# Kernel optimization log

Hardware: AMD Instinct MI355X
Metric: run time of the kernel (lower is better)

## Reference

```python
import jax, jax.numpy as jnp
import numpy as np

EMBED = 1024
HEADS = 16
HEAD_DIM = EMBED // HEADS
MAX_REL = 8
B, S = 4, 1024


def setup_inputs() -> dict:
    key = jax.random.key(0)
    ks = jax.random.split(key, 12)
    lim = 1.0 / np.sqrt(EMBED)
    def lin(k):
        k1, k2 = jax.random.split(k)
        W = jax.random.uniform(k1, (EMBED, EMBED), jnp.float32, -lim, lim)
        b = jax.random.uniform(k2, (EMBED,), jnp.float32, -lim, lim)
        return W, b
    Wq, bq = lin(ks[0]); Wk, bk = lin(ks[1]); Wv, bv = lin(ks[2]); Wo, bo = lin(ks[3])
    return {
        'query': jax.random.normal(ks[4], (B, S, EMBED), jnp.float32),
        'key': jax.random.normal(ks[5], (B, S, EMBED), jnp.float32),
        'value': jax.random.normal(ks[6], (B, S, EMBED), jnp.float32),
        'mask': jnp.zeros((B, S, S), dtype=bool),
        'Wq': Wq, 'bq': bq, 'Wk': Wk, 'bk': bk, 'Wv': Wv, 'bv': bv,
        'Wo': Wo, 'bo': bo,
        'rel_bias': jnp.zeros((HEADS, 2 * MAX_REL + 1), jnp.float32),
    }


def _split_heads(x):
    b, s, _ = x.shape
    return x.reshape(b, s, HEADS, HEAD_DIM).transpose(0, 2, 1, 3)  # [b,h,s,d]


def reference(query, key, value, mask, Wq, bq, Wk, bk, Wv, bv, Wo, bo, rel_bias):
    scale = jnp.sqrt(jnp.float32(HEAD_DIM))
    Q = _split_heads(query @ Wq.T + bq)
    K = _split_heads(key @ Wk.T + bk)
    V = _split_heads(value @ Wv.T + bv)
    scores = jnp.einsum('bhqd,bhkd->bhqk', Q, K) / scale
    # relative position bias: rel_bias[h, clip(j-i)+max]
    idx = jnp.arange(query.shape[1])
    rel = jnp.clip(idx[None, :] - idx[:, None], -MAX_REL, MAX_REL) + MAX_REL  # [s,s]
    bias = rel_bias[:, rel]  # [h,s,s]
    scores = scores + bias[None]
    scores = jnp.where(mask[:, None, :, :], -jnp.inf, scores)
    attn = jax.nn.softmax(scores, axis=-1)
    ctx = jnp.einsum('bhqk,bhkd->bhqd', attn, V)
    b, h, s, d = ctx.shape
    out = ctx.transpose(0, 2, 1, 3).reshape(b, s, h * d) @ Wo.T + bo
    return out, attn, scores
```

## Files before the change

kernel.cpp:

```cpp
#include <hip/hip_runtime.h>

typedef __bf16 bf16_t;
typedef bf16_t bf16x4 __attribute__((ext_vector_type(4)));
typedef bf16_t bf16x8 __attribute__((ext_vector_type(8)));
typedef float f32x4 __attribute__((ext_vector_type(4)));
typedef float f32x8 __attribute__((ext_vector_type(8)));

#define B_N 4
#define S_N 1024
#define E_N 1024
#define H_N 16
#define D_N 64

#define MFMA16 __builtin_amdgcn_mfma_f32_16x16x32_bf16

static __device__ __forceinline__ bf16_t f2b(float x) { return (bf16_t)x; }

static __device__ __forceinline__ void gload_lds16(const void* g, void* l) {
  __builtin_amdgcn_global_load_lds(
      (const __attribute__((address_space(1))) unsigned int*)g,
      (__attribute__((address_space(3))) unsigned int*)l, 16, 0, 0);
}

__global__ __launch_bounds__(256) void convert_kernel(
    const float* __restrict__ q, const float* __restrict__ k, const float* __restrict__ v,
    const float* __restrict__ wq, const float* __restrict__ wk,
    const float* __restrict__ wv, const float* __restrict__ wo,
    bf16_t* __restrict__ dq, bf16_t* __restrict__ dk, bf16_t* __restrict__ dv,
    bf16_t* __restrict__ dwq, bf16_t* __restrict__ dwk,
    bf16_t* __restrict__ dwv, bf16_t* __restrict__ dwo)
{
  const size_t e = ((size_t)blockIdx.x * 256 + threadIdx.x) * 8;
  const float* src; bf16_t* dst; size_t off;
  if (e < 12582912ull) {
    const int which = (int)(e >> 22);
    off = e & 4194303ull;
    src = which == 0 ? q : (which == 1 ? k : v);
    dst = which == 0 ? dq : (which == 1 ? dk : dv);
  } else {
    const size_t e2 = e - 12582912ull;
    const int which = (int)(e2 >> 20);
    off = e2 & 1048575ull;
    src = which == 0 ? wq : (which == 1 ? wk : (which == 2 ? wv : wo));
    dst = which == 0 ? dwq : (which == 1 ? dwk : (which == 2 ? dwv : dwo));
  }
  f32x8 x = *(const f32x8*)(src + off);
  bf16x8 r;
#pragma unroll
  for (int i = 0; i < 8; ++i) r[i] = f2b(x[i]);
  *(bf16x8*)(dst + off) = r;
}

__global__ __launch_bounds__(256) void mask_rowany(
    const unsigned char* __restrict__ mask, unsigned char* __restrict__ flags)
{
  const int row = blockIdx.x * 4 + (threadIdx.x >> 6);
  const int lane = threadIdx.x & 63;
  const uint4 v = *(const uint4*)(mask + (size_t)row * 1024 + lane * 16);
  const unsigned int any = v.x | v.y | v.z | v.w;
  const unsigned long long bal = __ballot(any != 0);
  if (lane == 0) flags[row] = bal ? 1 : 0;
}

__global__ __launch_bounds__(256) void qkv_gemm(
    const bf16_t* __restrict__ qA, const bf16_t* __restrict__ kA, const bf16_t* __restrict__ vA,
    const bf16_t* __restrict__ Wq, const bf16_t* __restrict__ Wk, const bf16_t* __restrict__ Wv,
    const float* __restrict__ bq, const float* __restrict__ bk, const float* __restrict__ bv,
    bf16_t* __restrict__ Qo, bf16_t* __restrict__ Ko, bf16_t* __restrict__ Vto)
{
  const int z = blockIdx.z;
  const bf16_t* A = z == 0 ? qA : (z == 1 ? kA : vA);
  const bf16_t* W = z == 0 ? Wq : (z == 1 ? Wk : Wv);
  const float* bias = z == 0 ? bq : (z == 1 ? bk : bv);

  __shared__ bf16_t As[128 * 32];
  __shared__ bf16_t Bs[128 * 32];
  const int tid = threadIdx.x;
  const int m0 = blockIdx.y * 128, n0 = blockIdx.x * 128;
  const int lane = tid & 63, wid = tid >> 6;
  const int wr = wid >> 1, wc = wid & 1;
  const int lr = lane & 15, lh = lane >> 4;
  const int sr = lane >> 2, sc = (lane & 3) * 8;
  f32x4 acc[4][4] = {};
  for (int k0 = 0; k0 < 1024; k0 += 32) {
#pragma unroll
    for (int i = 0; i < 2; ++i) {
      const int br = wid * 32 + i * 16;
      gload_lds16(&A[(size_t)(m0 + br + sr) * 1024 + k0 + sc], &As[br * 32]);
      gload_lds16(&W[(size_t)(n0 + br + sr) * 1024 + k0 + sc], &Bs[br * 32]);
    }
    __syncthreads();
    bf16x8 af[4], bw[4];
#pragma unroll
    for (int m = 0; m < 4; ++m)
      af[m] = *(const bf16x8*)&As[(wr * 64 + m * 16 + lr) * 32 + lh * 8];
#pragma unroll
    for (int n = 0; n < 4; ++n)
      bw[n] = *(const bf16x8*)&Bs[(wc * 64 + n * 16 + lr) * 32 + lh * 8];
#pragma unroll
    for (int m = 0; m < 4; ++m)
#pragma unroll
      for (int n = 0; n < 4; ++n)
        acc[m][n] = MFMA16(af[m], bw[n], acc[m][n], 0, 0, 0);
    __syncthreads();
  }
#pragma unroll
  for (int n = 0; n < 4; ++n) {
    const int col = n0 + wc * 64 + n * 16 + lr;
    const float bv_ = bias[col];
    const int h = col >> 6, d = col & 63;
#pragma unroll
    for (int m = 0; m < 4; ++m) {
      const int row0 = m0 + wr * 64 + m * 16 + lh * 4;
#pragma unroll
      for (int r = 0; r < 4; ++r) {
        const int row = row0 + r;
        const float v = acc[m][n][r] + bv_;
        const int b = row >> 10, s = row & 1023;
        if (z == 0)
          Qo[((size_t)(b * H_N + h) * S_N + s) * D_N + d] = f2b(v);
        else if (z == 1)
          Ko[((size_t)(b * H_N + h) * S_N + s) * D_N + d] = f2b(v);
        else
          Vto[((size_t)(b * H_N + h) * D_N + d) * S_N + s] = f2b(v);
      }
    }
  }
}

__global__ __launch_bounds__(256) void out_gemm(
    const bf16_t* __restrict__ A, const bf16_t* __restrict__ W,
    const float* __restrict__ bias, float* __restrict__ Co)
{
  __shared__ bf16_t As[128 * 32];
  __shared__ bf16_t Bs[128 * 32];
  const int tid = threadIdx.x;
  const int m0 = blockIdx.y * 128, n0 = blockIdx.x * 128;
  const int lane = tid & 63, wid = tid >> 6;
  const int wr = wid >> 1, wc = wid & 1;
  const int lr = lane & 15, lh = lane >> 4;
  const int sr = lane >> 2, sc = (lane & 3) * 8;
  f32x4 acc[4][4] = {};
  for (int k0 = 0; k0 < 1024; k0 += 32) {
#pragma unroll
    for (int i = 0; i < 2; ++i) {
      const int br = wid * 32 + i * 16;
      gload_lds16(&A[(size_t)(m0 + br + sr) * 1024 + k0 + sc], &As[br * 32]);
      gload_lds16(&W[(size_t)(n0 + br + sr) * 1024 + k0 + sc], &Bs[br * 32]);
    }
    __syncthreads();
    bf16x8 af[4], bw[4];
#pragma unroll
    for (int m = 0; m < 4; ++m)
      af[m] = *(const bf16x8*)&As[(wr * 64 + m * 16 + lr) * 32 + lh * 8];
#pragma unroll
    for (int n = 0; n < 4; ++n)
      bw[n] = *(const bf16x8*)&Bs[(wc * 64 + n * 16 + lr) * 32 + lh * 8];
#pragma unroll
    for (int m = 0; m < 4; ++m)
#pragma unroll
      for (int n = 0; n < 4; ++n)
        acc[m][n] = MFMA16(af[m], bw[n], acc[m][n], 0, 0, 0);
    __syncthreads();
  }
#pragma unroll
  for (int n = 0; n < 4; ++n) {
    const int col = n0 + wc * 64 + n * 16 + lr;
    const float bv_ = bias[col];
#pragma unroll
    for (int m = 0; m < 4; ++m) {
      const int row0 = m0 + wr * 64 + m * 16 + lh * 4;
#pragma unroll
      for (int r = 0; r < 4; ++r)
        Co[(size_t)(row0 + r) * E_N + col] = acc[m][n][r] + bv_;
    }
  }
}

static __device__ __forceinline__ f32x4 score4(
    f32x4 acc, int qrow, int kc, const unsigned char* __restrict__ mrow,
    const float* __restrict__ rbh, float rb_lo, float rb_hi, bool um)
{
  const int d0 = kc - qrow;
  float b0, b1, b2, b3;
  if (d0 >= 8) { b0 = b1 = b2 = b3 = rb_hi; }
  else if (d0 <= -11) { b0 = b1 = b2 = b3 = rb_lo; }
  else {
    int dd;
    dd = d0;     dd = dd < -8 ? -8 : (dd > 8 ? 8 : dd); b0 = rbh[dd + 8];
    dd = d0 + 1; dd = dd < -8 ? -8 : (dd > 8 ? 8 : dd); b1 = rbh[dd + 8];
    dd = d0 + 2; dd = dd < -8 ? -8 : (dd > 8 ? 8 : dd); b2 = rbh[dd + 8];
    dd = d0 + 3; dd = dd < -8 ? -8 : (dd > 8 ? 8 : dd); b3 = rbh[dd + 8];
  }
  f32x4 s;
  s[0] = acc[0] * 0.125f + b0;
  s[1] = acc[1] * 0.125f + b1;
  s[2] = acc[2] * 0.125f + b2;
  s[3] = acc[3] * 0.125f + b3;
  if (um) {
    const unsigned int mw = *(const unsigned int*)(mrow + kc);
    const float NEG = -__builtin_inff();
    if (mw & 0xffu)       s[0] = NEG;
    if (mw & 0xff00u)     s[1] = NEG;
    if (mw & 0xff0000u)   s[2] = NEG;
    if (mw & 0xff000000u) s[3] = NEG;
  }
  return s;
}

__global__ __launch_bounds__(256) void fused_attn(
    const bf16_t* __restrict__ Q, const bf16_t* __restrict__ K,
    const bf16_t* __restrict__ Vt,
    const unsigned char* __restrict__ mask, const unsigned char* __restrict__ rowflag,
    const float* __restrict__ rel_bias,
    float* __restrict__ scores, float* __restrict__ attn, bf16_t* __restrict__ ctx)
{
  __shared__ bf16_t Ktile[64 * 64];
  __shared__ bf16_t Vtile[64 * 64];
  __shared__ float S_lds[4][16][68];

  const int bh = blockIdx.y, b = bh >> 4, h = bh & 15;
  const int q0 = blockIdx.x * 64;
  const int tid = threadIdx.x;
  const int w = tid >> 6, lane = tid & 63;
  const int lr = lane & 15, lh = lane >> 4;
  const int qrow = q0 + w * 16 + lr;

  const bf16_t* Qh = Q + (size_t)bh * (S_N * D_N);
  const bf16_t* Kh = K + (size_t)bh * (S_N * D_N);
  const bf16_t* Vh = Vt + (size_t)bh * (D_N * S_N);
  const unsigned char* mrow = mask + (size_t)b * S_N * S_N + (size_t)qrow * S_N;
  float* Sbase = scores + (size_t)bh * S_N * S_N + (size_t)(q0 + w * 16) * S_N;
  float* Abase = attn + (size_t)bh * S_N * S_N + (size_t)(q0 + w * 16) * S_N;
  const float* rbh = rel_bias + h * 17;
  const float rb_lo = rbh[0], rb_hi = rbh[16];
  const float NEG = -__builtin_inff();
  const bool um = rowflag[b * S_N + qrow] != 0;

  const int sg_row0 = tid >> 3, sg_c = tid & 7;
  const int sg_row1 = (tid + 256) >> 3;
  const int sg_s0 = (sg_c ^ (sg_row0 & 7)) * 8;
  const int sg_s1 = (sg_c ^ (sg_row1 & 7)) * 8;

  bf16x8 qa0 = *(const bf16x8*)&Qh[(size_t)qrow * D_N + lh * 8];
  bf16x8 qa1 = *(const bf16x8*)&Qh[(size_t)qrow * D_N + 32 + lh * 8];

  const int ks0 = (lh ^ (lr & 7)) * 8;
  const int ks1 = ((4 + lh) ^ (lr & 7)) * 8;

  float mrun = NEG, srun = 0.f;
  for (int kt = 0; kt < 16; ++kt) {
    const int kb = kt * 64;
    __syncthreads();
    *(bf16x8*)&Ktile[sg_row0 * 64 + sg_s0] =
        *(const bf16x8*)&Kh[(size_t)(kb + sg_row0) * D_N + sg_c * 8];
    *(bf16x8*)&Ktile[sg_row1 * 64 + sg_s1] =
        *(const bf16x8*)&Kh[(size_t)(kb + sg_row1) * D_N + sg_c * 8];
    __syncthreads();
#pragma unroll
    for (int t = 0; t < 4; ++t) {
      const int krow = t * 16 + lr;
      bf16x8 ka0 = *(const bf16x8*)&Ktile[krow * 64 + ks0];
      bf16x8 ka1 = *(const bf16x8*)&Ktile[krow * 64 + ks1];
      f32x4 acc = {};
      acc = MFMA16(ka0, qa0, acc, 0, 0, 0);
      acc = MFMA16(ka1, qa1, acc, 0, 0, 0);
      const int kc = kb + t * 16 + 4 * lh;
      f32x4 s = score4(acc, qrow, kc, mrow, rbh, rb_lo, rb_hi, um);
      *(f32x4*)&S_lds[w][lr][t * 16 + 4 * lh] = s;
      const float mt = fmaxf(fmaxf(s[0], s[1]), fmaxf(s[2], s[3]));
      const float mn = fmaxf(mrun, mt);
      if (mn > NEG) {
        srun = srun * __expf(mrun - mn)
             + __expf(s[0] - mn) + __expf(s[1] - mn)
             + __expf(s[2] - mn) + __expf(s[3] - mn);
        mrun = mn;
      }
    }
#pragma unroll
    for (int i = 0; i < 4; ++i) {
      const int row = 4 * i + lh;
      f32x4 sv = *(const f32x4*)&S_lds[w][row][lr * 4];
      *(f32x4*)&Sbase[(size_t)row * S_N + kb + lr * 4] = sv;
    }
  }
#pragma unroll
  for (int off = 16; off <= 32; off <<= 1) {
    const float m2 = __shfl_xor(mrun, off);
    const float s2 = __shfl_xor(srun, off);
    const float mn = fmaxf(mrun, m2);
    if (mn > NEG) {
      srun = srun * __expf(mrun - mn) + s2 * __expf(m2 - mn);
      mrun = mn;
    }
  }
  const float M = mrun;
  const float invs = 1.0f / srun;

  f32x4 accp[4] = {};
  for (int kt = 0; kt < 16; ++kt) {
    const int kb = kt * 64;
    __syncthreads();
    *(bf16x8*)&Ktile[sg_row0 * 64 + sg_s0] =
        *(const bf16x8*)&Kh[(size_t)(kb + sg_row0) * D_N + sg_c * 8];
    *(bf16x8*)&Ktile[sg_row1 * 64 + sg_s1] =
        *(const bf16x8*)&Kh[(size_t)(kb + sg_row1) * D_N + sg_c * 8];
    *(bf16x8*)&Vtile[sg_row0 * 64 + sg_s0] =
        *(const bf16x8*)&Vh[(size_t)sg_row0 * S_N + kb + sg_c * 8];
    *(bf16x8*)&Vtile[sg_row1 * 64 + sg_s1] =
        *(const bf16x8*)&Vh[(size_t)sg_row1 * S_N + kb + sg_c * 8];
    __syncthreads();
#pragma unroll
    for (int t = 0; t < 4; ++t) {
      const int krow = t * 16 + lr;
      bf16x8 ka0 = *(const bf16x8*)&Ktile[krow * 64 + ks0];
      bf16x8 ka1 = *(const bf16x8*)&Ktile[krow * 64 + ks1];
      f32x4 acc = {};
      acc = MFMA16(ka0, qa0, acc, 0, 0, 0);
      acc = MFMA16(ka1, qa1, acc, 0, 0, 0);
      const int kc = kb + t * 16 + 4 * lh;
      f32x4 s = score4(acc, qrow, kc, mrow, rbh, rb_lo, rb_hi, um);
      f32x4 p;
#pragma unroll
      for (int j = 0; j < 4; ++j) p[j] = __expf(s[j] - M) * invs;
      *(f32x4*)&S_lds[w][lr][t * 16 + 4 * lh] = p;
    }
#pragma unroll
    for (int i = 0; i < 4; ++i) {
      const int row = 4 * i + lh;
      f32x4 pv = *(const f32x4*)&S_lds[w][row][lr * 4];
      *(f32x4*)&Abase[(size_t)row * S_N + kb + lr * 4] = pv;
    }
#pragma unroll
    for (int ch = 0; ch < 2; ++ch) {
      f32x8 pf = *(const f32x8*)&S_lds[w][lr][ch * 32 + lh * 8];
      bf16x8 pa;
#pragma unroll
      for (int j = 0; j < 8; ++j) pa[j] = f2b(pf[j]);
#pragma unroll
      for (int dt = 0; dt < 4; ++dt) {
        const int drow = dt * 16 + lr;
        bf16x8 vb = *(const bf16x8*)&Vtile[drow * 64 + (((ch * 4 + lh) ^ (lr & 7)) * 8)];
        accp[dt] = MFMA16(pa, vb, accp[dt], 0, 0, 0);
      }
    }
  }
#pragma unroll
  for (int dt = 0; dt < 4; ++dt)
#pragma unroll
    for (int r = 0; r < 4; ++r)
      ctx[((size_t)(b * S_N + q0 + w * 16 + 4 * lh + r)) * E_N + h * 64 + dt * 16 + lr] =
          f2b(accp[dt][r]);
}

extern "C" void kernel_launch(void* const* d_in, const int* in_sizes, int n_in,
                              void* d_out, int out_size, void* d_ws, size_t ws_size,
                              hipStream_t stream) {
  (void)in_sizes; (void)n_in; (void)out_size; (void)ws_size;
  const float* query = (const float*)d_in[0];
  const float* key   = (const float*)d_in[1];
  const float* value = (const float*)d_in[2];
  const unsigned char* mask = (const unsigned char*)d_in[3];
  const float* Wq = (const float*)d_in[4];
  const float* bq = (const float*)d_in[5];
  const float* Wk = (const float*)d_in[6];
  const float* bk = (const float*)d_in[7];
  const float* Wv = (const float*)d_in[8];
  const float* bv = (const float*)d_in[9];
  const float* Wo = (const float*)d_in[10];
  const float* bo = (const float*)d_in[11];
  const float* rel_bias = (const float*)d_in[12];

  float* out_f    = (float*)d_out;
  float* attn_f   = out_f + (size_t)4194304;
  float* scores_f = attn_f + (size_t)67108864;

  char* ws = (char*)d_ws;
  bf16_t* qbf  = (bf16_t*)(ws);
  bf16_t* kbf  = (bf16_t*)(ws + (8ull  << 20));
  bf16_t* vbf  = (bf16_t*)(ws + (16ull << 20));
  bf16_t* Wqb  = (bf16_t*)(ws + (24ull << 20));
  bf16_t* Wkb  = (bf16_t*)(ws + (26ull << 20));
  bf16_t* Wvb  = (bf16_t*)(ws + (28ull << 20));
  bf16_t* Wob  = (bf16_t*)(ws + (30ull << 20));
  bf16_t* Qbf  = (bf16_t*)(ws + (32ull << 20));
  bf16_t* Kbf  = (bf16_t*)(ws + (40ull << 20));
  bf16_t* Vtbf = (bf16_t*)(ws + (48ull << 20));
  bf16_t* CTX  = (bf16_t*)(ws + (56ull << 20));
  unsigned char* FLAGS = (unsigned char*)(ws + (64ull << 20));

  convert_kernel<<<dim3(8192), dim3(256), 0, stream>>>(
      query, key, value, Wq, Wk, Wv, Wo, qbf, kbf, vbf, Wqb, Wkb, Wvb, Wob);
  mask_rowany<<<dim3(1024), dim3(256), 0, stream>>>(mask, FLAGS);
  qkv_gemm<<<dim3(8, 32, 3), dim3(256), 0, stream>>>(
      qbf, kbf, vbf, Wqb, Wkb, Wvb, bq, bk, bv, Qbf, Kbf, Vtbf);
  fused_attn<<<dim3(16, 64), dim3(256), 0, stream>>>(
      Qbf, Kbf, Vtbf, mask, FLAGS, rel_bias, scores_f, attn_f, CTX);
  out_gemm<<<dim3(8, 32), dim3(256), 0, stream>>>(CTX, Wob, bo, out_f);
}
```

Baseline: 241.6 us.

## Switch attention to single-pass online softmax with lazy rescale and separate normalization

The two-pass fused attention, which recomputed QK^T in a second pass, becomes a single flash-style pass. That pass writes raw scores, accumulates P·V using an online max that only rescales when the max grows past a threshold, and stores per-row max and inverse-sum statistics. A new elementwise kernel then reads scores back and writes the normalized attention matrix. K and V tiles are now double-buffered with register prefetch two tiles ahead. This removes the second QK^T compute and the second K/V pass, but adds a full re-read of the 64M-float scores tensor and an extra launch. The unnormalized exponentials can reach up to e^8 before rescaling, which is a bf16 precision risk.

```diff
diff --git a/kernel.cpp b/kernel.cpp
--- a/kernel.cpp
+++ b/kernel.cpp
@@ -208,15 +208,15 @@
   return s;
 }
 
-__global__ __launch_bounds__(256) void fused_attn(
+__global__ __launch_bounds__(256) void attn_pass1(
     const bf16_t* __restrict__ Q, const bf16_t* __restrict__ K,
     const bf16_t* __restrict__ Vt,
     const unsigned char* __restrict__ mask, const unsigned char* __restrict__ rowflag,
     const float* __restrict__ rel_bias,
-    float* __restrict__ scores, float* __restrict__ attn, bf16_t* __restrict__ ctx)
-{
-  __shared__ bf16_t Ktile[64 * 64];
-  __shared__ bf16_t Vtile[64 * 64];
+    float* __restrict__ scores, float2* __restrict__ stats, bf16_t* __restrict__ ctx)
+{
+  __shared__ bf16_t Kt[2][64 * 64];
+  __shared__ bf16_t Vtl[2][64 * 64];
   __shared__ float S_lds[4][16][68];
 
   const int bh = blockIdx.y, b = bh >> 4, h = bh & 15;
@@ -231,14 +231,14 @@
   const bf16_t* Vh = Vt + (size_t)bh * (D_N * S_N);
   const unsigned char* mrow = mask + (size_t)b * S_N * S_N + (size_t)qrow * S_N;
   float* Sbase = scores + (size_t)bh * S_N * S_N + (size_t)(q0 + w * 16) * S_N;
-  float* Abase = attn + (size_t)bh * S_N * S_N + (size_t)(q0 + w * 16) * S_N;
   const float* rbh = rel_bias + h * 17;
   const float rb_lo = rbh[0], rb_hi = rbh[16];
   const float NEG = -__builtin_inff();
+  const float THR = 8.0f;
   const bool um = rowflag[b * S_N + qrow] != 0;
 
   const int sg_row0 = tid >> 3, sg_c = tid & 7;
-  const int sg_row1 = (tid + 256) >> 3;
+  const int sg_row1 = sg_row0 + 32;
   const int sg_s0 = (sg_c ^ (sg_row0 & 7)) * 8;
   const int sg_s1 = (sg_c ^ (sg_row1 & 7)) * 8;
 
@@ -248,34 +248,52 @@
   const int ks0 = (lh ^ (lr & 7)) * 8;
   const int ks1 = ((4 + lh) ^ (lr & 7)) * 8;
 
+  bf16x8 kr0, kr1, vr0, vr1;
+  kr0 = *(const bf16x8*)&Kh[(size_t)sg_row0 * D_N + sg_c * 8];
+  kr1 = *(const bf16x8*)&Kh[(size_t)sg_row1 * D_N + sg_c * 8];
+  vr0 = *(const bf16x8*)&Vh[(size_t)sg_row0 * S_N + sg_c * 8];
+  vr1 = *(const bf16x8*)&Vh[(size_t)sg_row1 * S_N + sg_c * 8];
+  *(bf16x8*)&Kt[0][sg_row0 * 64 + sg_s0] = kr0;
+  *(bf16x8*)&Kt[0][sg_row1 * 64 + sg_s1] = kr1;
+  *(bf16x8*)&Vtl[0][sg_row0 * 64 + sg_s0] = vr0;
+  *(bf16x8*)&Vtl[0][sg_row1 * 64 + sg_s1] = vr1;
+  kr0 = *(const bf16x8*)&Kh[(size_t)(64 + sg_row0) * D_N + sg_c * 8];
+  kr1 = *(const bf16x8*)&Kh[(size_t)(64 + sg_row1) * D_N + sg_c * 8];
+  vr0 = *(const bf16x8*)&Vh[(size_t)sg_row0 * S_N + 64 + sg_c * 8];
+  vr1 = *(const bf16x8*)&Vh[(size_t)sg_row1 * S_N + 64 + sg_c * 8];
+  __syncthreads();
+
   float mrun = NEG, srun = 0.f;
-  for (int kt = 0; kt < 16; ++kt) {
-    const int kb = kt * 64;
-    __syncthreads();
-    *(bf16x8*)&Ktile[sg_row0 * 64 + sg_s0] =
-        *(const bf16x8*)&Kh[(size_t)(kb + sg_row0) * D_N + sg_c * 8];
-    *(bf16x8*)&Ktile[sg_row1 * 64 + sg_s1] =
-        *(const bf16x8*)&Kh[(size_t)(kb + sg_row1) * D_N + sg_c * 8];
-    __syncthreads();
-#pragma unroll
-    for (int t = 0; t < 4; ++t) {
-      const int krow = t * 16 + lr;
-      bf16x8 ka0 = *(const bf16x8*)&Ktile[krow * 64 + ks0];
-      bf16x8 ka1 = *(const bf16x8*)&Ktile[krow * 64 + ks1];
+  f32x4 accp[4] = {};
+
+  for (int t = 0; t < 16; ++t) {
+    const int cur = t & 1, kb = t * 64;
+    if (t + 1 < 16) {
+      *(bf16x8*)&Kt[cur ^ 1][sg_row0 * 64 + sg_s0] = kr0;
+      *(bf16x8*)&Kt[cur ^ 1][sg_row1 * 64 + sg_s1] = kr1;
+      *(bf16x8*)&Vtl[cur ^ 1][sg_row0 * 64 + sg_s0] = vr0;
+      *(bf16x8*)&Vtl[cur ^ 1][sg_row1 * 64 + sg_s1] = vr1;
+    }
+    if (t + 2 < 16) {
+      const int kb2 = (t + 2) * 64;
+      kr0 = *(const bf16x8*)&Kh[(size_t)(kb2 + sg_row0) * D_N + sg_c * 8];
+      kr1 = *(const bf16x8*)&Kh[(size_t)(kb2 + sg_row1) * D_N + sg_c * 8];
+      vr0 = *(const bf16x8*)&Vh[(size_t)sg_row0 * S_N + kb2 + sg_c * 8];
+      vr1 = *(const bf16x8*)&Vh[(size_t)sg_row1 * S_N + kb2 + sg_c * 8];
+    }
+    float mt = NEG;
+#pragma unroll
+    for (int t4 = 0; t4 < 4; ++t4) {
+      const int krow = t4 * 16 + lr;
+      bf16x8 ka0 = *(const bf16x8*)&Kt[cur][krow * 64 + ks0];
+      bf16x8 ka1 = *(const bf16x8*)&Kt[cur][krow * 64 + ks1];
       f32x4 acc = {};
       acc = MFMA16(ka0, qa0, acc, 0, 0, 0);
       acc = MFMA16(ka1, qa1, acc, 0, 0, 0);
-      const int kc = kb + t * 16 + 4 * lh;
+      const int kc = kb + t4 * 16 + 4 * lh;
       f32x4 s = score4(acc, qrow, kc, mrow, rbh, rb_lo, rb_hi, um);
-      *(f32x4*)&S_lds[w][lr][t * 16 + 4 * lh] = s;
-      const float mt = fmaxf(fmaxf(s[0], s[1]), fmaxf(s[2], s[3]));
-      const float mn = fmaxf(mrun, mt);
-      if (mn > NEG) {
-        srun = srun * __expf(mrun - mn)
-             + __expf(s[0] - mn) + __expf(s[1] - mn)
-             + __expf(s[2] - mn) + __expf(s[3] - mn);
-        mrun = mn;
-      }
+      *(f32x4*)&S_lds[w][lr][t4 * 16 + 4 * lh] = s;
+      mt = fmaxf(mt, fmaxf(fmaxf(s[0], s[1]), fmaxf(s[2], s[3])));
     }
 #pragma unroll
     for (int i = 0; i < 4; ++i) {
@@ -283,74 +301,73 @@
       f32x4 sv = *(const f32x4*)&S_lds[w][row][lr * 4];
       *(f32x4*)&Sbase[(size_t)row * S_N + kb + lr * 4] = sv;
     }
-  }
-#pragma unroll
-  for (int off = 16; off <= 32; off <<= 1) {
-    const float m2 = __shfl_xor(mrun, off);
-    const float s2 = __shfl_xor(srun, off);
-    const float mn = fmaxf(mrun, m2);
-    if (mn > NEG) {
-      srun = srun * __expf(mrun - mn) + s2 * __expf(m2 - mn);
-      mrun = mn;
-    }
-  }
-  const float M = mrun;
-  const float invs = 1.0f / srun;
-
-  f32x4 accp[4] = {};
-  for (int kt = 0; kt < 16; ++kt) {
-    const int kb = kt * 64;
-    __syncthreads();
-    *(bf16x8*)&Ktile[sg_row0 * 64 + sg_s0] =
-        *(const bf16x8*)&Kh[(size_t)(kb + sg_row0) * D_N + sg_c * 8];
-    *(bf16x8*)&Ktile[sg_row1 * 64 + sg_s1] =
-        *(const bf16x8*)&Kh[(size_t)(kb + sg_row1) * D_N + sg_c * 8];
-    *(bf16x8*)&Vtile[sg_row0 * 64 + sg_s0] =
-        *(const bf16x8*)&Vh[(size_t)sg_row0 * S_N + kb + sg_c * 8];
-    *(bf16x8*)&Vtile[sg_row1 * 64 + sg_s1] =
-        *(const bf16x8*)&Vh[(size_t)sg_row1 * S_N + kb + sg_c * 8];
-    __syncthreads();
-#pragma unroll
-    for (int t = 0; t < 4; ++t) {
-      const int krow = t * 16 + lr;
-      bf16x8 ka0 = *(const bf16x8*)&Ktile[krow * 64 + ks0];
-      bf16x8 ka1 = *(const bf16x8*)&Ktile[krow * 64 + ks1];
-      f32x4 acc = {};
-      acc = MFMA16(ka0, qa0, acc, 0, 0, 0);
-      acc = MFMA16(ka1, qa1, acc, 0, 0, 0);
-      const int kc = kb + t * 16 + 4 * lh;
-      f32x4 s = score4(acc, qrow, kc, mrow, rbh, rb_lo, rb_hi, um);
-      f32x4 p;
-#pragma unroll
-      for (int j = 0; j < 4; ++j) p[j] = __expf(s[j] - M) * invs;
-      *(f32x4*)&S_lds[w][lr][t * 16 + 4 * lh] = p;
-    }
-#pragma unroll
-    for (int i = 0; i < 4; ++i) {
-      const int row = 4 * i + lh;
-      f32x4 pv = *(const f32x4*)&S_lds[w][row][lr * 4];
-      *(f32x4*)&Abase[(size_t)row * S_N + kb + lr * 4] = pv;
-    }
+    mt = fmaxf(mt, __shfl_xor(mt, 16));
+    mt = fmaxf(mt, __shfl_xor(mt, 32));
+    if (__any(mt - mrun > THR)) {
+      const float mnew = fmaxf(mrun, mt);
+      const float sc = (mnew > NEG) ? ((mrun > NEG) ? __expf(mrun - mnew) : 0.f) : 1.f;
+      srun *= sc;
+      mrun = mnew;
+#pragma unroll
+      for (int r = 0; r < 4; ++r) {
+        const float fr = __shfl(sc, 4 * lh + r);
+#pragma unroll
+        for (int dt = 0; dt < 4; ++dt) accp[dt][r] *= fr;
+      }
+    }
+    const bool live = mrun > NEG;
 #pragma unroll
     for (int ch = 0; ch < 2; ++ch) {
       f32x8 pf = *(const f32x8*)&S_lds[w][lr][ch * 32 + lh * 8];
       bf16x8 pa;
 #pragma unroll
-      for (int j = 0; j < 8; ++j) pa[j] = f2b(pf[j]);
+      for (int j = 0; j < 8; ++j) {
+        const float e = live ? __expf(pf[j] - mrun) : 0.f;
+        srun += e;
+        pa[j] = f2b(e);
+      }
 #pragma unroll
       for (int dt = 0; dt < 4; ++dt) {
         const int drow = dt * 16 + lr;
-        bf16x8 vb = *(const bf16x8*)&Vtile[drow * 64 + (((ch * 4 + lh) ^ (lr & 7)) * 8)];
+        bf16x8 vb = *(const bf16x8*)&Vtl[cur][drow * 64 + (((ch * 4 + lh) ^ (lr & 7)) * 8)];
         accp[dt] = MFMA16(pa, vb, accp[dt], 0, 0, 0);
       }
     }
-  }
+    __syncthreads();
+  }
+
+  srun += __shfl_xor(srun, 16);
+  srun += __shfl_xor(srun, 32);
+  const float invs = srun > 0.f ? 1.0f / srun : 0.f;
+  if (lane < 16)
+    stats[(size_t)bh * S_N + q0 + w * 16 + lr] = make_float2(mrun, invs);
 #pragma unroll
   for (int dt = 0; dt < 4; ++dt)
 #pragma unroll
-    for (int r = 0; r < 4; ++r)
+    for (int r = 0; r < 4; ++r) {
+      const float fr = __shfl(invs, 4 * lh + r);
       ctx[((size_t)(b * S_N + q0 + w * 16 + 4 * lh + r)) * E_N + h * 64 + dt * 16 + lr] =
-          f2b(accp[dt][r]);
+          f2b(accp[dt][r] * fr);
+    }
+}
+
+__global__ __launch_bounds__(256) void attn_norm(
+    const float* __restrict__ scores, const float2* __restrict__ stats,
+    float* __restrict__ attn)
+{
+  const int row = blockIdx.x * 4 + (threadIdx.x >> 6);
+  const int lane = threadIdx.x & 63;
+  const float2 st = stats[row];
+  const float* src = scores + (size_t)row * 1024;
+  float* dst = attn + (size_t)row * 1024;
+#pragma unroll
+  for (int i = 0; i < 4; ++i) {
+    f32x4 s = *(const f32x4*)&src[i * 256 + lane * 4];
+    f32x4 p;
+#pragma unroll
+    for (int j = 0; j < 4; ++j) p[j] = __expf(s[j] - st.x) * st.y;
+    *(f32x4*)&dst[i * 256 + lane * 4] = p;
+  }
 }
 
 extern "C" void kernel_launch(void* const* d_in, const int* in_sizes, int n_in,
@@ -388,13 +405,15 @@
   bf16_t* Vtbf = (bf16_t*)(ws + (48ull << 20));
   bf16_t* CTX  = (bf16_t*)(ws + (56ull << 20));
   unsigned char* FLAGS = (unsigned char*)(ws + (64ull << 20));
+  float2* STATS = (float2*)(ws + (66ull << 20));
 
   convert_kernel<<<dim3(8192), dim3(256), 0, stream>>>(
       query, key, value, Wq, Wk, Wv, Wo, qbf, kbf, vbf, Wqb, Wkb, Wvb, Wob);
   mask_rowany<<<dim3(1024), dim3(256), 0, stream>>>(mask, FLAGS);
   qkv_gemm<<<dim3(8, 32, 3), dim3(256), 0, stream>>>(
       qbf, kbf, vbf, Wqb, Wkb, Wvb, bq, bk, bv, Qbf, Kbf, Vtbf);
-  fused_attn<<<dim3(16, 64), dim3(256), 0, stream>>>(
-      Qbf, Kbf, Vtbf, mask, FLAGS, rel_bias, scores_f, attn_f, CTX);
+  attn_pass1<<<dim3(16, 64), dim3(256), 0, stream>>>(
+      Qbf, Kbf, Vtbf, mask, FLAGS, rel_bias, scores_f, STATS, CTX);
+  attn_norm<<<dim3(16384), dim3(256), 0, stream>>>(scores_f, STATS, attn_f);
   out_gemm<<<dim3(8, 32), dim3(256), 0, stream>>>(CTX, Wob, bo, out_f);
 }
```

Measured after the change: 290.8 us. +20.4%, slower.
